# Optimization experiments

Measured on AMD Instinct MI355X. Metric: run time of the kernel, lower is better.

## Reference

```python
import jax, jax.numpy as jnp
import numpy as np

N = 51200      # total nodes
G = 256        # graphs in batch
NPG = 200      # nodes per graph
E = 409600     # intra-graph edges
EPG = E // G
F_IN, HID, HEADS, NCLS = 768, 128, 4, 2


def setup_inputs() -> dict:
    key = jax.random.key(0)
    ks = jax.random.split(key, 20)
    x = jax.random.normal(ks[0], (N, F_IN), jnp.float32)
    # edges strictly inside each graph, no self-loops (PyG batching semantics)
    gid = jnp.arange(E, dtype=jnp.int32) // EPG
    sl = jax.random.randint(ks[1], (E,), 0, NPG, dtype=jnp.int32)
    off = jax.random.randint(ks[2], (E,), 1, NPG, dtype=jnp.int32)
    dl = (sl + off) % NPG
    edge_index = jnp.stack([gid * NPG + sl, gid * NPG + dl])
    batch = jnp.arange(N, dtype=jnp.int32) // NPG

    def glorot(k, shape, fan_in):
        return jax.random.normal(k, shape, jnp.float32) * np.float32(1.0 / np.sqrt(fan_in))

    return {
        'x': x, 'edge_index': edge_index, 'batch': batch,
        'W1': glorot(ks[3], (F_IN, HEADS * HID), F_IN),
        'a_src1': glorot(ks[4], (HEADS, HID), HID),
        'a_dst1': glorot(ks[5], (HEADS, HID), HID),
        'b1': jnp.zeros((HEADS * HID,), jnp.float32),
        'W2': glorot(ks[6], (HEADS * HID, HID), HEADS * HID),
        'a_src2': glorot(ks[7], (1, HID), HID),
        'a_dst2': glorot(ks[8], (1, HID), HID),
        'b2': jnp.zeros((HID,), jnp.float32),
        'Wc': glorot(ks[9], (HID, 2), HID),
        'bc': jnp.zeros((2,), jnp.float32),
        'Wf1': glorot(ks[10], (HID, HID), HID),
        'bf1': jnp.zeros((HID,), jnp.float32),
        'Wf2': glorot(ks[11], (HID, NCLS), HID),
        'bf2': jnp.zeros((NCLS,), jnp.float32),
    }


def _segment_softmax(logits, seg, num):
    m = jax.ops.segment_max(logits, seg, num_segments=num)
    e = jnp.exp(logits - m[seg])
    s = jax.ops.segment_sum(e, seg, num_segments=num)
    return e / (s[seg] + 1e-16)


def _gat(x, src, dst, W, a_s, a_d, b, n):
    # PyG GATConv, eval mode (attention dropout off), self-loops already in src/dst
    H, C = a_s.shape
    h = (x @ W).reshape(n, H, C)                       # [n,H,C]
    a_src = (h * a_s).sum(-1)                          # [n,H]
    a_dst = (h * a_d).sum(-1)
    logits = jax.nn.leaky_relu(a_src[src] + a_dst[dst], 0.2)  # [Etot,H]
    alpha = _segment_softmax(logits, dst, n)
    out = jax.ops.segment_sum(h[src] * alpha[:, :, None], dst, num_segments=n)
    return out.reshape(n, H * C) + b


def reference(x, edge_index, batch, W1, a_src1, a_dst1, b1, W2, a_src2, a_dst2, b2,
              Wc, bc, Wf1, bf1, Wf2, bf2):
    src0, dst0 = edge_index[0], edge_index[1]
    loop = jnp.arange(N, dtype=src0.dtype)
    src = jnp.concatenate([src0, loop])
    dst = jnp.concatenate([dst0, loop])

    h1 = jax.nn.relu(_gat(x, src, dst, W1, a_src1, a_dst1, b1, N))     # [N,512]
    h2 = jax.nn.relu(_gat(h1, src, dst, W2, a_src2, a_dst2, b2, N))    # [N,128]

    S = jax.nn.softmax(h2 @ Wc + bc, axis=1)                           # [N,2]

    # aggregate(): per-graph S^T A S via per-edge outer products (A from original edges)
    eg = batch[src0]
    outer = S[src0][:, :, None] * S[dst0][:, None, :]                  # [E,2,2]
    agg = jax.ops.segment_sum(outer, eg, num_segments=G)               # [G,2,2]
    rnorm = jnp.clip(jnp.abs(agg).sum(axis=2, keepdims=True), 1e-5, None)  # F.normalize p=1 dim=1
    nadj = agg / rnorm
    diag = jnp.diagonal(nadj, axis1=1, axis2=2)                        # [G,2]
    aggregate_loss = jnp.mean(jnp.mean((diag - 1.0) ** 2, axis=1))     # MSE vs ones, averaged over graphs

    # subgraph embedding: first row of S_g^T x_g per graph
    sub = jax.ops.segment_sum(S[:, 0:1] * h2, batch, num_segments=G)   # [G,128]

    out = jax.nn.relu(sub @ Wf1 + bf1)                                 # eval: dropout off
    out = out @ Wf2 + bf2                                              # [G,2]
    return out, aggregate_loss
```

## Files before the change

kernel.cpp:

```cpp
#include <hip/hip_runtime.h>
#include <hip/hip_bf16.h>
#include <cstdint>

#define N_NODES 51200
#define N_GRAPH 256
#define NPG     200
#define N_EDGE  409600
#define EPG     1600
#define F_IN    768
#define HID     128
#define HEADS   4
#define HC      512

typedef __attribute__((ext_vector_type(8))) short short8;
typedef __attribute__((ext_vector_type(4))) float floatx4;

constexpr size_t OFF_H1B    = 0;
constexpr size_t OFF_H2B    = OFF_H1B + (size_t)N_NODES * HC * 2;
constexpr size_t OFF_H2F    = OFF_H2B + (size_t)N_NODES * HID * 2;
constexpr size_t OFF_WT1    = OFF_H2F + (size_t)N_NODES * HID * 4;
constexpr size_t OFF_WT2    = OFF_WT1 + (size_t)HC * F_IN * 2;
constexpr size_t OFF_S      = OFF_WT2 + (size_t)HID * HC * 2;
constexpr size_t OFF_AGG    = OFF_S + (size_t)N_NODES * 2 * 4;
constexpr size_t OFF_SUB    = OFF_AGG + (size_t)N_GRAPH * 4 * 4;

__device__ __forceinline__ float leaky(float x) { return x >= 0.0f ? x : 0.2f * x; }

__device__ __forceinline__ unsigned short f2bf(float f) {
    unsigned int u = __float_as_uint(f);
    u += 0x7fffu + ((u >> 16) & 1u);
    return (unsigned short)(u >> 16);
}
__device__ __forceinline__ float bflo(int p) { return __uint_as_float((unsigned)p << 16); }
__device__ __forceinline__ float bfhi(int p) { return __uint_as_float((unsigned)p & 0xffff0000u); }

__device__ __forceinline__ void gl_lds16(const void* g, void* l) {
    __builtin_amdgcn_global_load_lds(
        (__attribute__((address_space(1))) void*)(g),
        (__attribute__((address_space(3))) void*)(l),
        16, 0, 0);
}

__global__ __launch_bounds__(256)
void transpose_cvt_kernel(const float* __restrict__ W, short* __restrict__ Wt,
                          int K, int Nn)
{
    int idx = blockIdx.x * 256 + threadIdx.x;
    if (idx >= K * Nn) return;
    int k = idx / Nn, n = idx % Nn;
    Wt[(size_t)n * K + k] = (short)f2bf(W[idx]);
}

template <bool A_BF16>
__global__ __launch_bounds__(256)
void gemm_mfma_kernel(const void* __restrict__ Av, const short* __restrict__ Bt,
                      unsigned short* __restrict__ C, int M, int Nn, int K)
{
    __shared__ __align__(16) short Ablob[4096];
    __shared__ __align__(16) short Bblob[4096];
    const int tid = threadIdx.x;
    const int w = tid >> 6, l = tid & 63;
    const int m0 = blockIdx.x * 128, n0 = blockIdx.y * 128;
    const int wr = w >> 1, wc = w & 1;

    floatx4 acc[4][4];
#pragma unroll
    for (int i = 0; i < 4; ++i)
#pragma unroll
        for (int j = 0; j < 4; ++j) acc[i][j] = (floatx4)0.0f;

    const short* bgp = Bt + (size_t)(n0 + (w * 2) * 16 + (l & 15)) * K + ((l >> 4) * 8);

    const float* Af = (const float*)Av;
    const short* Ab = (const short*)Av;
    const int r = tid >> 1, hh = tid & 1;
    const float* arow = Af + (size_t)(m0 + r) * K + hh * 16;
    const short* agp = Ab + (size_t)(m0 + (w * 2) * 16 + (l & 15)) * K + ((l >> 4) * 8);

    float4 pf0, pf1, pf2, pf3;
    if constexpr (!A_BF16) {
        pf0 = *(const float4*)(arow + 0);
        pf1 = *(const float4*)(arow + 4);
        pf2 = *(const float4*)(arow + 8);
        pf3 = *(const float4*)(arow + 12);
    }

    for (int k0 = 0; k0 < K; k0 += 32) {
        __syncthreads();
        if constexpr (A_BF16) {
            gl_lds16(agp + k0,          &Ablob[(w * 2) * 512]);
            gl_lds16(agp + 16 * K + k0, &Ablob[(w * 2 + 1) * 512]);
        } else {
            unsigned short us[16];
            us[0]=f2bf(pf0.x); us[1]=f2bf(pf0.y); us[2]=f2bf(pf0.z); us[3]=f2bf(pf0.w);
            us[4]=f2bf(pf1.x); us[5]=f2bf(pf1.y); us[6]=f2bf(pf1.z); us[7]=f2bf(pf1.w);
            us[8]=f2bf(pf2.x); us[9]=f2bf(pf2.y); us[10]=f2bf(pf2.z); us[11]=f2bf(pf2.w);
            us[12]=f2bf(pf3.x); us[13]=f2bf(pf3.y); us[14]=f2bf(pf3.z); us[15]=f2bf(pf3.w);
            const int o = (r >> 4) * 512 + (2 * hh) * 128 + (r & 15) * 8;
            short8 v0, v1;
#pragma unroll
            for (int j = 0; j < 8; ++j) { v0[j] = (short)us[j]; v1[j] = (short)us[8 + j]; }
            *(short8*)&Ablob[o]       = v0;
            *(short8*)&Ablob[o + 128] = v1;
        }
        gl_lds16(bgp + k0,          &Bblob[(w * 2) * 512]);
        gl_lds16(bgp + 16 * K + k0, &Bblob[(w * 2 + 1) * 512]);
        __syncthreads();

        if constexpr (!A_BF16) {
            if (k0 + 32 < K) {
                pf0 = *(const float4*)(arow + k0 + 32);
                pf1 = *(const float4*)(arow + k0 + 36);
                pf2 = *(const float4*)(arow + k0 + 40);
                pf3 = *(const float4*)(arow + k0 + 44);
            }
        }

        short8 af[4], bfr[4];
#pragma unroll
        for (int mi = 0; mi < 4; ++mi)
            af[mi] = *(const short8*)&Ablob[(wr * 4 + mi) * 512 + l * 8];
#pragma unroll
        for (int ni = 0; ni < 4; ++ni)
            bfr[ni] = *(const short8*)&Bblob[(wc * 4 + ni) * 512 + l * 8];
#pragma unroll
        for (int mi = 0; mi < 4; ++mi)
#pragma unroll
            for (int ni = 0; ni < 4; ++ni)
                acc[mi][ni] = __builtin_amdgcn_mfma_f32_16x16x32_bf16(
                    af[mi], bfr[ni], acc[mi][ni], 0, 0, 0);
    }

    const int lr = (l >> 4) * 4, lc = l & 15;
#pragma unroll
    for (int mi = 0; mi < 4; ++mi)
#pragma unroll
        for (int ni = 0; ni < 4; ++ni) {
            const size_t base = (size_t)(m0 + wr * 64 + mi * 16 + lr) * Nn
                              + (n0 + wc * 64 + ni * 16 + lc);
#pragma unroll
            for (int rr = 0; rr < 4; ++rr)
                C[base + (size_t)rr * Nn] = f2bf(acc[mi][ni][rr]);
        }
}

__global__ __launch_bounds__(512)
void gat1_kernel(const unsigned short* __restrict__ H, const int* __restrict__ src0,
                 const int* __restrict__ dst0, const float* __restrict__ a_s,
                 const float* __restrict__ a_d, const float* __restrict__ b1,
                 unsigned short* __restrict__ out)
{
    const int g = blockIdx.x, h = blockIdx.y;
    __shared__ int   s_feat[NPG * 64];
    __shared__ float s_as[NPG], s_ad[NPG], s_m[NPG], s_inv[NPG];
    __shared__ int   s_row[NPG + 1];
    __shared__ int   s_cnt[NPG];
    __shared__ int   s_scan[256];
    __shared__ unsigned short s_eraw[EPG];
    __shared__ int2  s_wc[EPG];
    const int tid = threadIdx.x, w = tid >> 6, l = tid & 63;
    const int gbase = g * NPG;

    for (int flat = tid; flat < NPG * 16; flat += 512) {
        int row = flat >> 4, q = flat & 15;
        uint4 v = *(const uint4*)(H + (size_t)(gbase + row) * HC + h * HID + q * 8);
        *(uint4*)&s_feat[row * 64 + q * 4] = v;
    }
    for (int j = tid; j < EPG; j += 512) {
        int s = src0[g * EPG + j] - gbase;
        int d = dst0[g * EPG + j] - gbase;
        s_eraw[j] = (unsigned short)(s | (d << 8));
    }
    if (tid < NPG) s_cnt[tid] = 0;
    __syncthreads();

    for (int j = tid; j < EPG; j += 512)
        atomicAdd(&s_cnt[s_eraw[j] >> 8], 1);
    const float2 av = ((const float2*)(a_s + h * HID))[l];
    const float2 dv = ((const float2*)(a_d + h * HID))[l];
    for (int nl = w; nl < NPG; nl += 8) {
        int pk = s_feat[nl * 64 + l];
        float f0 = bflo(pk), f1 = bfhi(pk);
        float ss = f0 * av.x + f1 * av.y;
        float sd = f0 * dv.x + f1 * dv.y;
#pragma unroll
        for (int off = 1; off < 64; off <<= 1) {
            ss += __shfl_xor(ss, off);
            sd += __shfl_xor(sd, off);
        }
        if (l == 0) { s_as[nl] = ss; s_ad[nl] = sd; }
    }
    __syncthreads();

    {
        int v = (tid < NPG) ? s_cnt[tid] : 0;
        if (tid < 256) s_scan[tid] = v;
        __syncthreads();
        for (int off = 1; off < 256; off <<= 1) {
            int u = (tid >= off && tid < 256) ? s_scan[tid - off] : 0;
            __syncthreads();
            if (tid < 256) s_scan[tid] += u;
            __syncthreads();
        }
        if (tid < NPG) s_row[tid + 1] = s_scan[tid];
        if (tid == 0) s_row[0] = 0;
        __syncthreads();
        if (tid < NPG) s_scan[tid] = s_row[tid];
    }
    __syncthreads();

    for (int j = tid; j < EPG; j += 512) {
        int pk = s_eraw[j];
        int p = atomicAdd(&s_scan[pk >> 8], 1);
        s_wc[p].y = pk;
    }
    __syncthreads();

    for (int j = tid; j < EPG; j += 512) {
        int pk = s_wc[j].y;
        s_wc[j].x = __float_as_int(leaky(s_as[pk & 255] + s_ad[pk >> 8]));
    }
    __syncthreads();

    if (tid < NPG) {
        float m = leaky(s_as[tid] + s_ad[tid]);
        int r0 = s_row[tid], r1 = s_row[tid + 1];
        for (int j = r0; j < r1; ++j) m = fmaxf(m, __int_as_float(s_wc[j].x));
        s_m[tid] = m;
    }
    __syncthreads();

    for (int j = tid; j < EPG; j += 512) {
        int2 e = s_wc[j];
        s_wc[j].x = __float_as_int(__expf(__int_as_float(e.x) - s_m[e.y >> 8]));
    }
    __syncthreads();

    if (tid < NPG) {
        float rs = __expf(leaky(s_as[tid] + s_ad[tid]) - s_m[tid]);
        int r0 = s_row[tid], r1 = s_row[tid + 1];
        for (int j = r0; j < r1; ++j) rs += __int_as_float(s_wc[j].x);
        s_inv[tid] = 1.0f / (rs + 1e-16f);
    }
    __syncthreads();

    const float2 bv = ((const float2*)(b1 + h * HID))[l];
    for (int nl = w; nl < NPG; nl += 8) {
        const int r0 = s_row[nl], r1 = s_row[nl + 1];
        const float wself = __expf(leaky(s_as[nl] + s_ad[nl]) - s_m[nl]);
        int spk = s_feat[nl * 64 + l];
        float a0 = wself * bflo(spk), a1 = wself * bfhi(spk);
        float c0 = 0.0f, c1 = 0.0f;
        int j = r0;
        for (; j + 4 <= r1; j += 4) {
            int2 e0 = s_wc[j], e1 = s_wc[j + 1], e2 = s_wc[j + 2], e3 = s_wc[j + 3];
            int p0 = s_feat[(e0.y & 255) * 64 + l];
            int p1 = s_feat[(e1.y & 255) * 64 + l];
            int p2 = s_feat[(e2.y & 255) * 64 + l];
            int p3 = s_feat[(e3.y & 255) * 64 + l];
            float w0 = __int_as_float(e0.x), w1 = __int_as_float(e1.x);
            float w2 = __int_as_float(e2.x), w3 = __int_as_float(e3.x);
            a0 += w0 * bflo(p0); a1 += w0 * bfhi(p0);
            c0 += w1 * bflo(p1); c1 += w1 * bfhi(p1);
            a0 += w2 * bflo(p2); a1 += w2 * bfhi(p2);
            c0 += w3 * bflo(p3); c1 += w3 * bfhi(p3);
        }
        for (; j < r1; ++j) {
            int2 e0 = s_wc[j];
            int p0 = s_feat[(e0.y & 255) * 64 + l];
            float w0 = __int_as_float(e0.x);
            a0 += w0 * bflo(p0); a1 += w0 * bfhi(p0);
        }
        const float inv = s_inv[nl];
        float o0 = (a0 + c0) * inv + bv.x;
        float o1 = (a1 + c1) * inv + bv.y;
        unsigned int st = (unsigned int)f2bf(fmaxf(o0, 0.0f))
                        | ((unsigned int)f2bf(fmaxf(o1, 0.0f)) << 16);
        *(unsigned int*)&out[(size_t)(gbase + nl) * HC + h * HID + 2 * l] = st;
    }
}

__global__ __launch_bounds__(512)
void gat2_kernel(const unsigned short* __restrict__ H, const int* __restrict__ src0,
                 const int* __restrict__ dst0, const float* __restrict__ a_s,
                 const float* __restrict__ a_d, const float* __restrict__ b2,
                 const float* __restrict__ Wc, const float* __restrict__ bc,
                 float* __restrict__ h2, float* __restrict__ S)
{
    const int g = blockIdx.x;
    __shared__ int   s_feat[NPG * 64];
    __shared__ float s_as[NPG], s_ad[NPG], s_m[NPG], s_inv[NPG];
    __shared__ int   s_row[NPG + 1];
    __shared__ int   s_cnt[NPG];
    __shared__ int   s_scan[256];
    __shared__ unsigned short s_eraw[EPG];
    __shared__ int2  s_wc[EPG];
    const int tid = threadIdx.x, w = tid >> 6, l = tid & 63;
    const int gbase = g * NPG;

    for (int flat = tid; flat < NPG * 16; flat += 512) {
        int row = flat >> 4, q = flat & 15;
        uint4 v = *(const uint4*)(H + (size_t)(gbase + row) * HID + q * 8);
        *(uint4*)&s_feat[row * 64 + q * 4] = v;
    }
    for (int j = tid; j < EPG; j += 512) {
        int s = src0[g * EPG + j] - gbase;
        int d = dst0[g * EPG + j] - gbase;
        s_eraw[j] = (unsigned short)(s | (d << 8));
    }
    if (tid < NPG) s_cnt[tid] = 0;
    __syncthreads();

    for (int j = tid; j < EPG; j += 512)
        atomicAdd(&s_cnt[s_eraw[j] >> 8], 1);
    const float2 av = ((const float2*)a_s)[l];
    const float2 dv = ((const float2*)a_d)[l];
    for (int nl = w; nl < NPG; nl += 8) {
        int pk = s_feat[nl * 64 + l];
        float f0 = bflo(pk), f1 = bfhi(pk);
        float ss = f0 * av.x + f1 * av.y;
        float sd = f0 * dv.x + f1 * dv.y;
#pragma unroll
        for (int off = 1; off < 64; off <<= 1) {
            ss += __shfl_xor(ss, off);
            sd += __shfl_xor(sd, off);
        }
        if (l == 0) { s_as[nl] = ss; s_ad[nl] = sd; }
    }
    __syncthreads();

    {
        int v = (tid < NPG) ? s_cnt[tid] : 0;
        if (tid < 256) s_scan[tid] = v;
        __syncthreads();
        for (int off = 1; off < 256; off <<= 1) {
            int u = (tid >= off && tid < 256) ? s_scan[tid - off] : 0;
            __syncthreads();
            if (tid < 256) s_scan[tid] += u;
            __syncthreads();
        }
        if (tid < NPG) s_row[tid + 1] = s_scan[tid];
        if (tid == 0) s_row[0] = 0;
        __syncthreads();
        if (tid < NPG) s_scan[tid] = s_row[tid];
    }
    __syncthreads();

    for (int j = tid; j < EPG; j += 512) {
        int pk = s_eraw[j];
        int p = atomicAdd(&s_scan[pk >> 8], 1);
        s_wc[p].y = pk;
    }
    __syncthreads();

    for (int j = tid; j < EPG; j += 512) {
        int pk = s_wc[j].y;
        s_wc[j].x = __float_as_int(leaky(s_as[pk & 255] + s_ad[pk >> 8]));
    }
    __syncthreads();

    if (tid < NPG) {
        float m = leaky(s_as[tid] + s_ad[tid]);
        int r0 = s_row[tid], r1 = s_row[tid + 1];
        for (int j = r0; j < r1; ++j) m = fmaxf(m, __int_as_float(s_wc[j].x));
        s_m[tid] = m;
    }
    __syncthreads();

    for (int j = tid; j < EPG; j += 512) {
        int2 e = s_wc[j];
        s_wc[j].x = __float_as_int(__expf(__int_as_float(e.x) - s_m[e.y >> 8]));
    }
    __syncthreads();

    if (tid < NPG) {
        float rs = __expf(leaky(s_as[tid] + s_ad[tid]) - s_m[tid]);
        int r0 = s_row[tid], r1 = s_row[tid + 1];
        for (int j = r0; j < r1; ++j) rs += __int_as_float(s_wc[j].x);
        s_inv[tid] = 1.0f / (rs + 1e-16f);
    }
    __syncthreads();

    const float2 bv = ((const float2*)b2)[l];
    const float4 wcv = ((const float4*)Wc)[l];
    const float bc0 = bc[0], bc1 = bc[1];
    for (int nl = w; nl < NPG; nl += 8) {
        const int r0 = s_row[nl], r1 = s_row[nl + 1];
        const float wself = __expf(leaky(s_as[nl] + s_ad[nl]) - s_m[nl]);
        int spk = s_feat[nl * 64 + l];
        float a0 = wself * bflo(spk), a1 = wself * bfhi(spk);
        float c0 = 0.0f, c1 = 0.0f;
        int j = r0;
        for (; j + 4 <= r1; j += 4) {
            int2 e0 = s_wc[j], e1 = s_wc[j + 1], e2 = s_wc[j + 2], e3 = s_wc[j + 3];
            int p0 = s_feat[(e0.y & 255) * 64 + l];
            int p1 = s_feat[(e1.y & 255) * 64 + l];
            int p2 = s_feat[(e2.y & 255) * 64 + l];
            int p3 = s_feat[(e3.y & 255) * 64 + l];
            float w0 = __int_as_float(e0.x), w1 = __int_as_float(e1.x);
            float w2 = __int_as_float(e2.x), w3 = __int_as_float(e3.x);
            a0 += w0 * bflo(p0); a1 += w0 * bfhi(p0);
            c0 += w1 * bflo(p1); c1 += w1 * bfhi(p1);
            a0 += w2 * bflo(p2); a1 += w2 * bfhi(p2);
            c0 += w3 * bflo(p3); c1 += w3 * bfhi(p3);
        }
        for (; j < r1; ++j) {
            int2 e0 = s_wc[j];
            int p0 = s_feat[(e0.y & 255) * 64 + l];
            float w0 = __int_as_float(e0.x);
            a0 += w0 * bflo(p0); a1 += w0 * bfhi(p0);
        }
        const float inv = s_inv[nl];
        float o0 = fmaxf((a0 + c0) * inv + bv.x, 0.0f);
        float o1 = fmaxf((a1 + c1) * inv + bv.y, 0.0f);
        *(float2*)&h2[(size_t)(gbase + nl) * HID + 2 * l] = make_float2(o0, o1);
        float z0 = o0 * wcv.x + o1 * wcv.z;
        float z1 = o0 * wcv.y + o1 * wcv.w;
#pragma unroll
        for (int off = 1; off < 64; off <<= 1) {
            z0 += __shfl_xor(z0, off);
            z1 += __shfl_xor(z1, off);
        }
        if (l == 0) {
            z0 += bc0; z1 += bc1;
            float mm = fmaxf(z0, z1);
            float e0 = __expf(z0 - mm), e1 = __expf(z1 - mm);
            float is = 1.0f / (e0 + e1);
            *(float2*)&S[(size_t)(gbase + nl) * 2] = make_float2(e0 * is, e1 * is);
        }
    }
}

__global__ __launch_bounds__(256)
void agg_kernel(const int* __restrict__ src0, const int* __restrict__ dst0,
                const float* __restrict__ S, float* __restrict__ agg)
{
    const int g = blockIdx.x, tid = threadIdx.x;
    float a00 = 0, a01 = 0, a10 = 0, a11 = 0;
    for (int e = g*EPG + tid; e < (g + 1)*EPG; e += 256) {
        int s = src0[e], d = dst0[e];
        float s0 = S[s*2], s1 = S[s*2 + 1];
        float d0 = S[d*2], d1 = S[d*2 + 1];
        a00 += s0*d0; a01 += s0*d1; a10 += s1*d0; a11 += s1*d1;
    }
    for (int off = 32; off > 0; off >>= 1) {
        a00 += __shfl_down(a00, off); a01 += __shfl_down(a01, off);
        a10 += __shfl_down(a10, off); a11 += __shfl_down(a11, off);
    }
    __shared__ float sred[4][4];
    if ((tid & 63) == 0) {
        int w = tid >> 6;
        sred[w][0] = a00; sred[w][1] = a01; sred[w][2] = a10; sred[w][3] = a11;
    }
    __syncthreads();
    if (tid == 0) {
        agg[g*4 + 0] = sred[0][0] + sred[1][0] + sred[2][0] + sred[3][0];
        agg[g*4 + 1] = sred[0][1] + sred[1][1] + sred[2][1] + sred[3][1];
        agg[g*4 + 2] = sred[0][2] + sred[1][2] + sred[2][2] + sred[3][2];
        agg[g*4 + 3] = sred[0][3] + sred[1][3] + sred[2][3] + sred[3][3];
    }
}

__global__ __launch_bounds__(256)
void loss_kernel(const float* __restrict__ agg, float* __restrict__ out_loss)
{
    int tid = threadIdx.x;
    float a00 = agg[tid*4 + 0], a01 = agg[tid*4 + 1];
    float a10 = agg[tid*4 + 2], a11 = agg[tid*4 + 3];
    float rn0 = fmaxf(fabsf(a00) + fabsf(a01), 1e-5f);
    float rn1 = fmaxf(fabsf(a10) + fabsf(a11), 1e-5f);
    float d0 = a00 / rn0 - 1.0f, d1 = a11 / rn1 - 1.0f;
    float contrib = 0.5f * (d0*d0 + d1*d1);
    for (int off = 32; off > 0; off >>= 1) contrib += __shfl_down(contrib, off);
    __shared__ float sred[4];
    if ((tid & 63) == 0) sred[tid >> 6] = contrib;
    __syncthreads();
    if (tid == 0)
        out_loss[0] = (sred[0] + sred[1] + sred[2] + sred[3]) * (1.0f / N_GRAPH);
}

__global__ __launch_bounds__(128)
void sub_kernel(const float* __restrict__ S, const float* __restrict__ h2,
                float* __restrict__ sub)
{
    const int g = blockIdx.x, c = threadIdx.x;
    const float* Sg = S + (size_t)g * NPG * 2;
    const float* hg = h2 + (size_t)g * NPG * HID;
    float acc = 0.0f;
    for (int i = 0; i < NPG; ++i)
        acc += Sg[i*2] * hg[(size_t)i*HID + c];
    sub[g*HID + c] = acc;
}

__global__ __launch_bounds__(128)
void final_kernel(const float* __restrict__ sub, const float* __restrict__ Wf1,
                  const float* __restrict__ bf1, const float* __restrict__ Wf2,
                  const float* __restrict__ bf2, float* __restrict__ out)
{
    __shared__ float s_sub[128];
    __shared__ float s_fc[128];
    const int g = blockIdx.x, t = threadIdx.x;
    s_sub[t] = sub[g*HID + t];
    __syncthreads();
    float acc = bf1[t];
    for (int c = 0; c < 128; ++c)
        acc += s_sub[c] * Wf1[c*128 + t];
    s_fc[t] = fmaxf(acc, 0.0f);
    __syncthreads();
    if (t < 2) {
        float z = bf2[t];
        for (int j = 0; j < 128; ++j) z += s_fc[j] * Wf2[j*2 + t];
        out[g*2 + t] = z;
    }
}

extern "C" void kernel_launch(void* const* d_in, const int* in_sizes, int n_in,
                              void* d_out, int out_size, void* d_ws, size_t ws_size,
                              hipStream_t stream)
{
    const float* x   = (const float*)d_in[0];
    const int*   ei  = (const int*)d_in[1];
    const float* W1  = (const float*)d_in[3];
    const float* as1 = (const float*)d_in[4];
    const float* ad1 = (const float*)d_in[5];
    const float* b1  = (const float*)d_in[6];
    const float* W2  = (const float*)d_in[7];
    const float* as2 = (const float*)d_in[8];
    const float* ad2 = (const float*)d_in[9];
    const float* b2  = (const float*)d_in[10];
    const float* Wc  = (const float*)d_in[11];
    const float* bc  = (const float*)d_in[12];
    const float* Wf1 = (const float*)d_in[13];
    const float* bf1 = (const float*)d_in[14];
    const float* Wf2 = (const float*)d_in[15];
    const float* bf2 = (const float*)d_in[16];
    const int* src0 = ei;
    const int* dst0 = ei + N_EDGE;

    char* ws = (char*)d_ws;
    unsigned short* H1b = (unsigned short*)(ws + OFF_H1B);
    unsigned short* H2b = (unsigned short*)(ws + OFF_H2B);
    float* h2    = (float*)(ws + OFF_H2F);
    short* Wt1   = (short*)(ws + OFF_WT1);
    short* Wt2   = (short*)(ws + OFF_WT2);
    float* Sbuf  = (float*)(ws + OFF_S);
    float* aggb  = (float*)(ws + OFF_AGG);
    float* subb  = (float*)(ws + OFF_SUB);
    float* out   = (float*)d_out;

    transpose_cvt_kernel<<<(F_IN*HC + 255)/256, 256, 0, stream>>>(W1, Wt1, F_IN, HC);
    transpose_cvt_kernel<<<(HC*HID + 255)/256, 256, 0, stream>>>(W2, Wt2, HC, HID);

    gemm_mfma_kernel<false><<<dim3(N_NODES/128, HC/128), 256, 0, stream>>>(
        x, Wt1, H1b, N_NODES, HC, F_IN);

    gat1_kernel<<<dim3(N_GRAPH, HEADS), 512, 0, stream>>>(
        H1b, src0, dst0, as1, ad1, b1, H1b);

    gemm_mfma_kernel<true><<<dim3(N_NODES/128, HID/128), 256, 0, stream>>>(
        H1b, Wt2, H2b, N_NODES, HID, HC);

    gat2_kernel<<<N_GRAPH, 512, 0, stream>>>(
        H2b, src0, dst0, as2, ad2, b2, Wc, bc, h2, Sbuf);

    agg_kernel<<<N_GRAPH, 256, 0, stream>>>(src0, dst0, Sbuf, aggb);
    loss_kernel<<<1, 256, 0, stream>>>(aggb, out + N_GRAPH*2);

    sub_kernel<<<N_GRAPH, 128, 0, stream>>>(Sbuf, h2, subb);
    final_kernel<<<N_GRAPH, 128, 0, stream>>>(subb, Wf1, bf1, Wf2, bf2, out);

    (void)in_sizes; (void)n_in; (void)out_size; (void)ws_size;
}
```

Measured before the change: 512.4 us.

## Double-buffer GEMM LDS tiles, remap workgroups by XCD, use packed bf16 convert

The MFMA GEMM now uses two LDS buffers, so the next K-tile loads and the fp32-to-bf16 conversion overlap with the current tile's MFMAs, and there is one barrier per iteration instead of two. The 2D grid becomes 1D with a swizzle that spreads consecutive workgroups across the 8 XCDs and maps each to an M/N tile, aiming for better L2 reuse of the B operand. Conversion switches to the packed v_cvt_pk_bf16_f32 instruction. LDS use doubles and register pressure rises from the two-deep A prefetch. The swizzle assumes the grid size is divisible by 8.

```diff
diff --git a/kernel.cpp b/kernel.cpp
--- a/kernel.cpp
+++ b/kernel.cpp
@@ -34,6 +34,12 @@
 __device__ __forceinline__ float bflo(int p) { return __uint_as_float((unsigned)p << 16); }
 __device__ __forceinline__ float bfhi(int p) { return __uint_as_float((unsigned)p & 0xffff0000u); }
 
+__device__ __forceinline__ unsigned int cvtpk(float lo, float hi) {
+    unsigned int r;
+    asm("v_cvt_pk_bf16_f32 %0, %1, %2" : "=v"(r) : "v"(lo), "v"(hi));
+    return r;
+}
+
 __device__ __forceinline__ void gl_lds16(const void* g, void* l) {
     __builtin_amdgcn_global_load_lds(
         (__attribute__((address_space(1))) void*)(g),
@@ -41,6 +47,16 @@
         16, 0, 0);
 }
 
+__device__ __forceinline__ void store_cvt(short* dst, float4 a, float4 b, float4 c, float4 d) {
+    uint4 q0, q1;
+    q0.x = cvtpk(a.x, a.y); q0.y = cvtpk(a.z, a.w);
+    q0.z = cvtpk(b.x, b.y); q0.w = cvtpk(b.z, b.w);
+    q1.x = cvtpk(c.x, c.y); q1.y = cvtpk(c.z, c.w);
+    q1.z = cvtpk(d.x, d.y); q1.w = cvtpk(d.z, d.w);
+    *(uint4*)dst = q0;
+    *(uint4*)(dst + 128) = q1;
+}
+
 __global__ __launch_bounds__(256)
 void transpose_cvt_kernel(const float* __restrict__ W, short* __restrict__ Wt,
                           int K, int Nn)
@@ -56,11 +72,17 @@
 void gemm_mfma_kernel(const void* __restrict__ Av, const short* __restrict__ Bt,
                       unsigned short* __restrict__ C, int M, int Nn, int K)
 {
-    __shared__ __align__(16) short Ablob[4096];
-    __shared__ __align__(16) short Bblob[4096];
+    __shared__ __align__(16) short Ablob[2][4096];
+    __shared__ __align__(16) short Bblob[2][4096];
     const int tid = threadIdx.x;
     const int w = tid >> 6, l = tid & 63;
-    const int m0 = blockIdx.x * 128, n0 = blockIdx.y * 128;
+
+    const int nwg = gridDim.x;
+    int wg = blockIdx.x;
+    wg = (wg & 7) * (nwg >> 3) + (wg >> 3);
+    const int nbx = Nn >> 7;
+    const int m0 = (wg / nbx) * 128;
+    const int n0 = (wg % nbx) * 128;
     const int wr = w >> 1, wc = w & 1;
 
     floatx4 acc[4][4];
@@ -76,59 +98,79 @@
     const int r = tid >> 1, hh = tid & 1;
     const float* arow = Af + (size_t)(m0 + r) * K + hh * 16;
     const short* agp = Ab + (size_t)(m0 + (w * 2) * 16 + (l & 15)) * K + ((l >> 4) * 8);
-
-    float4 pf0, pf1, pf2, pf3;
+    const int oA = (r >> 4) * 512 + (2 * hh) * 128 + (r & 15) * 8;
+
+    const int nt = K >> 5;
+
+    if constexpr (A_BF16) {
+        gl_lds16(agp,            &Ablob[0][(w * 2) * 512]);
+        gl_lds16(agp + 16 * K,   &Ablob[0][(w * 2 + 1) * 512]);
+    }
+    gl_lds16(bgp,            &Bblob[0][(w * 2) * 512]);
+    gl_lds16(bgp + 16 * K,   &Bblob[0][(w * 2 + 1) * 512]);
+
+    float4 pA0 = {}, pA1 = {}, pA2 = {}, pA3 = {};
+    float4 pB0 = {}, pB1 = {}, pB2 = {}, pB3 = {};
     if constexpr (!A_BF16) {
-        pf0 = *(const float4*)(arow + 0);
-        pf1 = *(const float4*)(arow + 4);
-        pf2 = *(const float4*)(arow + 8);
-        pf3 = *(const float4*)(arow + 12);
-    }
-
-    for (int k0 = 0; k0 < K; k0 += 32) {
-        __syncthreads();
-        if constexpr (A_BF16) {
-            gl_lds16(agp + k0,          &Ablob[(w * 2) * 512]);
-            gl_lds16(agp + 16 * K + k0, &Ablob[(w * 2 + 1) * 512]);
-        } else {
-            unsigned short us[16];
-            us[0]=f2bf(pf0.x); us[1]=f2bf(pf0.y); us[2]=f2bf(pf0.z); us[3]=f2bf(pf0.w);
-            us[4]=f2bf(pf1.x); us[5]=f2bf(pf1.y); us[6]=f2bf(pf1.z); us[7]=f2bf(pf1.w);
-            us[8]=f2bf(pf2.x); us[9]=f2bf(pf2.y); us[10]=f2bf(pf2.z); us[11]=f2bf(pf2.w);
-            us[12]=f2bf(pf3.x); us[13]=f2bf(pf3.y); us[14]=f2bf(pf3.z); us[15]=f2bf(pf3.w);
-            const int o = (r >> 4) * 512 + (2 * hh) * 128 + (r & 15) * 8;
-            short8 v0, v1;
-#pragma unroll
-            for (int j = 0; j < 8; ++j) { v0[j] = (short)us[j]; v1[j] = (short)us[8 + j]; }
-            *(short8*)&Ablob[o]       = v0;
-            *(short8*)&Ablob[o + 128] = v1;
-        }
-        gl_lds16(bgp + k0,          &Bblob[(w * 2) * 512]);
-        gl_lds16(bgp + 16 * K + k0, &Bblob[(w * 2 + 1) * 512]);
-        __syncthreads();
-
+        float4 c0 = *(const float4*)(arow + 0);
+        float4 c1 = *(const float4*)(arow + 4);
+        float4 c2 = *(const float4*)(arow + 8);
+        float4 c3 = *(const float4*)(arow + 12);
+        store_cvt(&Ablob[0][oA], c0, c1, c2, c3);
+        if (nt > 1) {
+            pA0 = *(const float4*)(arow + 32);
+            pA1 = *(const float4*)(arow + 36);
+            pA2 = *(const float4*)(arow + 40);
+            pA3 = *(const float4*)(arow + 44);
+        }
+    }
+    __syncthreads();
+
+    for (int t = 0; t < nt; ++t) {
+        const int cur = t & 1, nxt = cur ^ 1;
+        const int kn = (t + 1) << 5;
+
+        if (t + 1 < nt) {
+            gl_lds16(bgp + kn,            &Bblob[nxt][(w * 2) * 512]);
+            gl_lds16(bgp + 16 * K + kn,   &Bblob[nxt][(w * 2 + 1) * 512]);
+            if constexpr (A_BF16) {
+                gl_lds16(agp + kn,          &Ablob[nxt][(w * 2) * 512]);
+                gl_lds16(agp + 16 * K + kn, &Ablob[nxt][(w * 2 + 1) * 512]);
+            }
+        }
         if constexpr (!A_BF16) {
-            if (k0 + 32 < K) {
-                pf0 = *(const float4*)(arow + k0 + 32);
-                pf1 = *(const float4*)(arow + k0 + 36);
-                pf2 = *(const float4*)(arow + k0 + 40);
-                pf3 = *(const float4*)(arow + k0 + 44);
+            if (t + 2 < nt) {
+                const float* ap = arow + ((t + 2) << 5);
+                pB0 = *(const float4*)(ap + 0);
+                pB1 = *(const float4*)(ap + 4);
+                pB2 = *(const float4*)(ap + 8);
+                pB3 = *(const float4*)(ap + 12);
             }
         }
 
         short8 af[4], bfr[4];
 #pragma unroll
         for (int mi = 0; mi < 4; ++mi)
-            af[mi] = *(const short8*)&Ablob[(wr * 4 + mi) * 512 + l * 8];
+            af[mi] = *(const short8*)&Ablob[cur][(wr * 4 + mi) * 512 + l * 8];
 #pragma unroll
         for (int ni = 0; ni < 4; ++ni)
-            bfr[ni] = *(const short8*)&Bblob[(wc * 4 + ni) * 512 + l * 8];
+            bfr[ni] = *(const short8*)&Bblob[cur][(wc * 4 + ni) * 512 + l * 8];
 #pragma unroll
         for (int mi = 0; mi < 4; ++mi)
 #pragma unroll
             for (int ni = 0; ni < 4; ++ni)
                 acc[mi][ni] = __builtin_amdgcn_mfma_f32_16x16x32_bf16(
                     af[mi], bfr[ni], acc[mi][ni], 0, 0, 0);
+
+        if constexpr (!A_BF16) {
+            if (t + 1 < nt) {
+                store_cvt(&Ablob[nxt][oA], pA0, pA1, pA2, pA3);
+            }
+            if (t + 2 < nt) {
+                pA0 = pB0; pA1 = pB1; pA2 = pB2; pA3 = pB3;
+            }
+        }
+        __syncthreads();
     }
 
     const int lr = (l >> 4) * 4, lc = l & 15;
@@ -551,13 +593,13 @@
     transpose_cvt_kernel<<<(F_IN*HC + 255)/256, 256, 0, stream>>>(W1, Wt1, F_IN, HC);
     transpose_cvt_kernel<<<(HC*HID + 255)/256, 256, 0, stream>>>(W2, Wt2, HC, HID);
 
-    gemm_mfma_kernel<false><<<dim3(N_NODES/128, HC/128), 256, 0, stream>>>(
+    gemm_mfma_kernel<false><<<(N_NODES/128) * (HC/128), 256, 0, stream>>>(
         x, Wt1, H1b, N_NODES, HC, F_IN);
 
     gat1_kernel<<<dim3(N_GRAPH, HEADS), 512, 0, stream>>>(
         H1b, src0, dst0, as1, ad1, b1, H1b);
 
-    gemm_mfma_kernel<true><<<dim3(N_NODES/128, HID/128), 256, 0, stream>>>(
+    gemm_mfma_kernel<true><<<(N_NODES/128) * (HID/128), 256, 0, stream>>>(
         H1b, Wt2, H2b, N_NODES, HID, HC);
 
     gat2_kernel<<<N_GRAPH, 512, 0, stream>>>(
```

Result: faster. 498.0 us (-2.8%).
